# Performance work log

Measured on AMD Instinct MI355X. Metric: run time of the kernel, lower is better.

Reference implementation:

```python
import jax, jax.numpy as jnp
import numpy as np

B, S, D, H, L = 8, 4096, 512, 512, 2


def log_g(x):
    # log of g(x) where g(x) = x + 0.5 for x >= 0 else sigmoid(x)
    return jnp.where(x >= 0, jnp.log(jax.nn.relu(x) + 0.5), -jax.nn.softplus(-x))


def g(x):
    return jnp.where(x >= 0, x + 0.5, jax.nn.sigmoid(x))


def mingru_layer(x, h0, wz, bz, wh, bh):
    """Log-space parallel-scan minGRU layer.
    x: (B,S,Din), h0: (B,1,H) positive (already g-activated).
    wz,wh: (H,Din); bz,bh: (H,). Returns full hidden sequence (B,S,H)."""
    k = jnp.einsum('bsd,hd->bsh', x, wz) + bz          # gate pre-activation
    log_z = -jax.nn.softplus(-k)                        # log sigmoid(k)
    log_coeffs = -jax.nn.softplus(k)                    # log(1 - sigmoid(k))
    log_h_tilde = log_g(jnp.einsum('bsd,hd->bsh', x, wh) + bh)
    log_values = log_z + log_h_tilde                    # log(z * h_tilde)
    log_h0 = jnp.log(h0)                                # (B,1,H)
    # Heinsen associative scan in log space
    a_star = jnp.cumsum(
        jnp.concatenate([jnp.zeros_like(log_h0), log_coeffs], axis=1), axis=1)  # (B,S+1,H)
    log_vals = jnp.concatenate([log_h0, log_values], axis=1)                     # (B,S+1,H)
    log_h = a_star + jax.lax.cumlogsumexp(log_vals - a_star, axis=1)
    return jnp.exp(log_h)[:, 1:]                        # (B,S,H)


def setup_inputs() -> dict:
    key = jax.random.key(0)
    ks = jax.random.split(key, 1 + 4 * L)
    x = jax.random.normal(ks[0], (B, S, D), dtype=jnp.float32)
    inp = {'x': x}
    dims_in = [D] + [H] * (L - 1)
    i = 1
    for l in range(L):
        din = dims_in[l]
        stdv = 1.0 / np.sqrt(din)
        inp[f'wz{l}'] = jax.random.uniform(ks[i], (H, din), minval=-stdv, maxval=stdv); i += 1
        inp[f'bz{l}'] = jax.random.uniform(ks[i], (H,), minval=-stdv, maxval=stdv); i += 1
        inp[f'wh{l}'] = jax.random.uniform(ks[i], (H, din), minval=-stdv, maxval=stdv); i += 1
        inp[f'bh{l}'] = jax.random.uniform(ks[i], (H,), minval=-stdv, maxval=stdv); i += 1
    return inp


def reference(x, wz0, bz0, wh0, bh0, wz1, bz1, wh1, bh1):
    # h is None -> h0 = g(zeros) = 0.5 for every layer
    h0 = jnp.full((B, 1, H), 0.5, dtype=x.dtype)
    params = [(wz0, bz0, wh0, bh0), (wz1, bz1, wh1, bh1)]
    inp = x
    finals = []
    for (wz, bz, wh, bh) in params:
        out = mingru_layer(inp, h0, wz, bz, wh, bh)
        finals.append(out[:, -1:])
        inp = out  # Identity layer transform, no residual, dropout=0
    return out, jnp.stack(finals)  # (B,S,H), (L,B,1,H)
```

## Files before the change

kernel.cpp:

```cpp
#include <hip/hip_runtime.h>
#include <math.h>

#define BB 8
#define SS 4096
#define DD 512
#define HH 512
#define MM (BB*SS)

constexpr int TCH = 64;
constexpr int NC  = SS / TCH;
constexpr int BH  = BB * HH;

constexpr int BM = 128;
constexpr int BN = 64;
constexpr int BK = 64;

typedef short  short8  __attribute__((ext_vector_type(8)));
typedef float  float4v __attribute__((ext_vector_type(4)));

__device__ inline unsigned short f2bf(float f) {
    union { float f; unsigned u; } v; v.f = f;
    unsigned r = v.u + 0x7FFF + ((v.u >> 16) & 1);
    return (unsigned short)(r >> 16);
}
__device__ inline float bf_lo(unsigned u) {
    union { unsigned u; float f; } x; x.u = u << 16; return x.f;
}
__device__ inline float bf_hi(unsigned u) {
    union { unsigned u; float f; } x; x.u = u & 0xffff0000u; return x.f;
}

__device__ inline void async_copy16(const void* g, void* l) {
    __builtin_amdgcn_global_load_lds(
        (const __attribute__((address_space(1))) void*)g,
        (__attribute__((address_space(3))) void*)l, 16, 0, 0);
}

__global__ __launch_bounds__(256)
void conv_bf16(const float* __restrict__ in, short* __restrict__ out) {
    const size_t base = ((size_t)blockIdx.x * 256 + threadIdx.x) * 8;
    float4 a = *(const float4*)(in + base);
    float4 b = *(const float4*)(in + base + 4);
    short8 r;
    r[0] = f2bf(a.x); r[1] = f2bf(a.y); r[2] = f2bf(a.z); r[3] = f2bf(a.w);
    r[4] = f2bf(b.x); r[5] = f2bf(b.y); r[6] = f2bf(b.z); r[7] = f2bf(b.w);
    *(short8*)(out + base) = r;
}

__global__ __launch_bounds__(256)
void conv_bf16_w4(const float* __restrict__ w0, const float* __restrict__ w1,
                  const float* __restrict__ w2, const float* __restrict__ w3,
                  short* __restrict__ out) {
    const float* src = (blockIdx.y == 0) ? w0 : (blockIdx.y == 1) ? w1
                     : (blockIdx.y == 2) ? w2 : w3;
    const size_t base = ((size_t)blockIdx.x * 256 + threadIdx.x) * 8;
    float4 a = *(const float4*)(src + base);
    float4 b = *(const float4*)(src + base + 4);
    short8 r;
    r[0] = f2bf(a.x); r[1] = f2bf(a.y); r[2] = f2bf(a.z); r[3] = f2bf(a.w);
    r[4] = f2bf(b.x); r[5] = f2bf(b.y); r[6] = f2bf(b.z); r[7] = f2bf(b.w);
    *(short8*)(out + (size_t)blockIdx.y * HH * DD + base) = r;
}

__global__ __launch_bounds__(256)
void gemm_gate_mfma(const short* __restrict__ Xg, const short* __restrict__ Wz,
                    const float* __restrict__ bz, const short* __restrict__ Wh,
                    const float* __restrict__ bh, unsigned* __restrict__ AV,
                    float2* __restrict__ cAV)
{
    __shared__ char smem[32768];
    short*    lds    = (short*)smem;
    unsigned* lds_av = (unsigned*)smem;
    constexpr int ZOFF = BM * BK;
    constexpr int HOFF = BM * BK + BN * BK;

    const int t    = threadIdx.x;
    const int wave = t >> 6;
    const int lane = t & 63;
    const int col16 = lane & 15;
    const int quad  = lane >> 4;
    const int wm = wave >> 1;
    const int wn = wave & 1;
    const int m0 = blockIdx.x * BM;
    const int n0 = blockIdx.y * BN;

    float4v accz[4][2], acch[4][2];
    #pragma unroll
    for (int i = 0; i < 4; ++i)
        #pragma unroll
        for (int j = 0; j < 2; ++j) {
            accz[i][j] = (float4v){0.f, 0.f, 0.f, 0.f};
            acch[i][j] = (float4v){0.f, 0.f, 0.f, 0.f};
        }

    const int lr = lane >> 3;
    const int lc = (lane & 7) * 8;

    for (int k0 = 0; k0 < DD; k0 += BK) {
        #pragma unroll
        for (int i = 0; i < 4; ++i) {
            const int r0 = wave * 32 + i * 8;
            async_copy16(Xg + (size_t)(m0 + r0 + lr) * DD + k0 + lc,
                         &lds[r0 * BK]);
        }
        #pragma unroll
        for (int i = 0; i < 2; ++i) {
            const int r0 = wave * 16 + i * 8;
            async_copy16(Wz + (size_t)(n0 + r0 + lr) * DD + k0 + lc,
                         &lds[ZOFF + r0 * BK]);
            async_copy16(Wh + (size_t)(n0 + r0 + lr) * DD + k0 + lc,
                         &lds[HOFF + r0 * BK]);
        }
        __syncthreads();

        #pragma unroll
        for (int kk = 0; kk < 2; ++kk) {
            short8 af[4], bzf[2], bhf[2];
            #pragma unroll
            for (int mi = 0; mi < 4; ++mi)
                af[mi] = *(const short8*)&lds[(wm*64 + mi*16 + col16) * BK + kk*32 + quad*8];
            #pragma unroll
            for (int nj = 0; nj < 2; ++nj) {
                bzf[nj] = *(const short8*)&lds[ZOFF + (wn*32 + nj*16 + col16) * BK + kk*32 + quad*8];
                bhf[nj] = *(const short8*)&lds[HOFF + (wn*32 + nj*16 + col16) * BK + kk*32 + quad*8];
            }
            #pragma unroll
            for (int mi = 0; mi < 4; ++mi)
                #pragma unroll
                for (int nj = 0; nj < 2; ++nj) {
                    accz[mi][nj] = __builtin_amdgcn_mfma_f32_16x16x32_bf16(af[mi], bzf[nj], accz[mi][nj], 0, 0, 0);
                    acch[mi][nj] = __builtin_amdgcn_mfma_f32_16x16x32_bf16(af[mi], bhf[nj], acch[mi][nj], 0, 0, 0);
                }
        }
        __syncthreads();
    }

    #pragma unroll
    for (int nj = 0; nj < 2; ++nj) {
        const int ln = wn*32 + nj*16 + col16;
        const int n  = n0 + ln;
        const float bzn = bz[n], bhn = bh[n];
        #pragma unroll
        for (int mi = 0; mi < 4; ++mi) {
            const int lmb = wm*64 + mi*16 + quad*4;
            #pragma unroll
            for (int reg = 0; reg < 4; ++reg) {
                const float kz = accz[mi][nj][reg] + bzn;
                const float kh = acch[mi][nj][reg] + bhn;
                const float a  = 1.0f / (1.0f + __expf(kz));
                const float ht = (kh >= 0.0f) ? (kh + 0.5f)
                                              : (1.0f / (1.0f + __expf(-kh)));
                const float v  = (1.0f - a) * ht;
                lds_av[(lmb + reg) * 64 + ln] = ((unsigned)f2bf(v) << 16) | f2bf(a);
            }
        }
    }
    __syncthreads();

    {
        const int row0 = t >> 4;
        const int col  = (t & 15) * 4;
        #pragma unroll
        for (int i = 0; i < 8; ++i) {
            const int row = row0 + i * 16;
            const uint4 u = *(const uint4*)&lds_av[row * 64 + col];
            *(uint4*)&AV[(size_t)(m0 + row) * HH + n0 + col] = u;
        }
    }

    if (t < 128) {
        const int c  = t >> 6;
        const int ln = t & 63;
        float prod = 1.0f, hl = 0.0f;
        #pragma unroll 8
        for (int s = 0; s < TCH; ++s) {
            const unsigned u = lds_av[(c * TCH + s) * 64 + ln];
            const float a = bf_lo(u), v = bf_hi(u);
            hl   = fmaf(a, hl, v);
            prod *= a;
        }
        const int b  = m0 >> 12;
        const int cg = ((m0 & 4095) >> 6) + c;
        cAV[(size_t)cg * BH + b * HH + (n0 + ln)] = make_float2(prod, hl);
    }
}

__global__ __launch_bounds__(256)
void scan_apply_f32(const unsigned* __restrict__ AV,
                    const float2* __restrict__ cAV,
                    float* __restrict__ out, float* __restrict__ finals)
{
    const int h = blockIdx.x * 256 + threadIdx.x;
    const int b = blockIdx.y;
    const int c = blockIdx.z;
    const int ch = b * HH + h;
    float hcur = 0.5f;
    for (int cp = 0; cp < c; ++cp) {
        const float2 s = cAV[(size_t)cp * BH + ch];
        hcur = fmaf(s.x, hcur, s.y);
    }
    size_t base = ((size_t)(b * SS + c * TCH)) * HH + h;
    for (int tt = 0; tt < TCH; ++tt) {
        const unsigned u = AV[base];
        hcur = fmaf(bf_lo(u), hcur, bf_hi(u));
        out[base] = hcur;
        base += HH;
    }
    if (c == NC - 1) finals[ch] = hcur;
}

__global__ __launch_bounds__(256)
void scan_apply_bf16(const unsigned* __restrict__ AV,
                     const float2* __restrict__ cAV,
                     short* __restrict__ out, float* __restrict__ finals)
{
    const int h = blockIdx.x * 256 + threadIdx.x;
    const int b = blockIdx.y;
    const int c = blockIdx.z;
    const int ch = b * HH + h;
    float hcur = 0.5f;
    for (int cp = 0; cp < c; ++cp) {
        const float2 s = cAV[(size_t)cp * BH + ch];
        hcur = fmaf(s.x, hcur, s.y);
    }
    size_t base = ((size_t)(b * SS + c * TCH)) * HH + h;
    for (int tt = 0; tt < TCH; ++tt) {
        const unsigned u = AV[base];
        hcur = fmaf(bf_lo(u), hcur, bf_hi(u));
        out[base] = (short)f2bf(hcur);
        base += HH;
    }
    if (c == NC - 1) finals[ch] = hcur;
}

extern "C" void kernel_launch(void* const* d_in, const int* in_sizes, int n_in,
                              void* d_out, int out_size, void* d_ws, size_t ws_size,
                              hipStream_t stream)
{
    const float* x   = (const float*)d_in[0];
    const float* wz0 = (const float*)d_in[1];
    const float* bz0 = (const float*)d_in[2];
    const float* wh0 = (const float*)d_in[3];
    const float* bh0 = (const float*)d_in[4];
    const float* wz1 = (const float*)d_in[5];
    const float* bz1 = (const float*)d_in[6];
    const float* wh1 = (const float*)d_in[7];
    const float* bh1 = (const float*)d_in[8];

    float* out    = (float*)d_out;
    float* finals = out + (size_t)MM * HH;

    unsigned* AV  = (unsigned*)d_ws;
    short* Xbf    = (short*)(AV + (size_t)MM * HH);
    short* Wbf    = Xbf + (size_t)MM * DD;
    float2* cAV   = (float2*)(Wbf + (size_t)4 * HH * DD);

    short* Wz0 = Wbf;
    short* Wh0 = Wbf + (size_t)1 * HH * DD;
    short* Wz1 = Wbf + (size_t)2 * HH * DD;
    short* Wh1 = Wbf + (size_t)3 * HH * DD;

    const dim3 gg(MM / BM, HH / BN);
    const dim3 gs(HH / 256, BB, NC);

    conv_bf16   <<<MM * DD / 8 / 256, 256, 0, stream>>>(x, Xbf);
    conv_bf16_w4<<<dim3(HH * DD / 8 / 256, 4), 256, 0, stream>>>(wz0, wh0, wz1, wh1, Wbf);

    gemm_gate_mfma <<<gg, 256, 0, stream>>>(Xbf, Wz0, bz0, Wh0, bh0, AV, cAV);
    scan_apply_bf16<<<gs, 256, 0, stream>>>(AV, cAV, Xbf, finals);

    gemm_gate_mfma <<<gg, 256, 0, stream>>>(Xbf, Wz1, bz1, Wh1, bh1, AV, cAV);
    scan_apply_f32 <<<gs, 256, 0, stream>>>(AV, cAV, out, finals + BH);
}
```

Measured before the change: 332.4 us.

## Merge conversion kernels, use fast reciprocal, split chunk reduction across all threads

Merges the x and weight bf16 conversion kernels into one launch to save a kernel launch. In the GEMM epilogue, exact divisions are replaced with the hardware reciprocal, and the sigmoid is evaluated without a branch. The per-chunk prefix reduction now uses all 256 threads: each half-chunk is reduced separately and the two are combined with a lane shuffle, which halves the serial loop length. The scan loops also get an unroll pragma. The reciprocal approximation may slightly change numerics.

```diff
diff --git a/kernel.cpp b/kernel.cpp
--- a/kernel.cpp
+++ b/kernel.cpp
@@ -29,6 +29,9 @@
 __device__ inline float bf_hi(unsigned u) {
     union { unsigned u; float f; } x; x.u = u & 0xffff0000u; return x.f;
 }
+__device__ inline float fast_rcp(float x) {
+    return __builtin_amdgcn_rcpf(x);
+}
 
 __device__ inline void async_copy16(const void* g, void* l) {
     __builtin_amdgcn_global_load_lds(
@@ -37,29 +40,31 @@
 }
 
 __global__ __launch_bounds__(256)
-void conv_bf16(const float* __restrict__ in, short* __restrict__ out) {
-    const size_t base = ((size_t)blockIdx.x * 256 + threadIdx.x) * 8;
-    float4 a = *(const float4*)(in + base);
-    float4 b = *(const float4*)(in + base + 4);
-    short8 r;
-    r[0] = f2bf(a.x); r[1] = f2bf(a.y); r[2] = f2bf(a.z); r[3] = f2bf(a.w);
-    r[4] = f2bf(b.x); r[5] = f2bf(b.y); r[6] = f2bf(b.z); r[7] = f2bf(b.w);
-    *(short8*)(out + base) = r;
-}
-
-__global__ __launch_bounds__(256)
-void conv_bf16_w4(const float* __restrict__ w0, const float* __restrict__ w1,
-                  const float* __restrict__ w2, const float* __restrict__ w3,
-                  short* __restrict__ out) {
-    const float* src = (blockIdx.y == 0) ? w0 : (blockIdx.y == 1) ? w1
-                     : (blockIdx.y == 2) ? w2 : w3;
-    const size_t base = ((size_t)blockIdx.x * 256 + threadIdx.x) * 8;
+void conv_all(const float* __restrict__ x,
+              const float* __restrict__ w0, const float* __restrict__ w1,
+              const float* __restrict__ w2, const float* __restrict__ w3,
+              short* __restrict__ Xbf, short* __restrict__ Wbf)
+{
+    constexpr int XBLK = MM * DD / 8 / 256;
+    constexpr int WBLK = HH * DD / 8 / 256;
+    const int bid = blockIdx.x;
+    const float* src; short* dst; size_t base;
+    if (bid < XBLK) {
+        src = x; dst = Xbf;
+        base = ((size_t)bid * 256 + threadIdx.x) * 8;
+    } else {
+        const int idx  = bid - XBLK;
+        const int wsel = idx / WBLK;
+        src = (wsel == 0) ? w0 : (wsel == 1) ? w1 : (wsel == 2) ? w2 : w3;
+        dst = Wbf + (size_t)wsel * HH * DD;
+        base = ((size_t)(idx % WBLK) * 256 + threadIdx.x) * 8;
+    }
     float4 a = *(const float4*)(src + base);
     float4 b = *(const float4*)(src + base + 4);
     short8 r;
     r[0] = f2bf(a.x); r[1] = f2bf(a.y); r[2] = f2bf(a.z); r[3] = f2bf(a.w);
     r[4] = f2bf(b.x); r[5] = f2bf(b.y); r[6] = f2bf(b.z); r[7] = f2bf(b.w);
-    *(short8*)(out + (size_t)blockIdx.y * HH * DD + base) = r;
+    *(short8*)(dst + base) = r;
 }
 
 __global__ __launch_bounds__(256)
@@ -147,9 +152,9 @@
             for (int reg = 0; reg < 4; ++reg) {
                 const float kz = accz[mi][nj][reg] + bzn;
                 const float kh = acch[mi][nj][reg] + bhn;
-                const float a  = 1.0f / (1.0f + __expf(kz));
-                const float ht = (kh >= 0.0f) ? (kh + 0.5f)
-                                              : (1.0f / (1.0f + __expf(-kh)));
+                const float a  = fast_rcp(1.0f + __expf(kz));
+                const float sn = fast_rcp(1.0f + __expf(-kh));
+                const float ht = (kh >= 0.0f) ? (kh + 0.5f) : sn;
                 const float v  = (1.0f - a) * ht;
                 lds_av[(lmb + reg) * 64 + ln] = ((unsigned)f2bf(v) << 16) | f2bf(a);
             }
@@ -168,20 +173,27 @@
         }
     }
 
-    if (t < 128) {
-        const int c  = t >> 6;
-        const int ln = t & 63;
+    {
+        const int task = t >> 1;
+        const int hf   = t & 1;
+        const int c    = task >> 6;
+        const int ln   = task & 63;
         float prod = 1.0f, hl = 0.0f;
         #pragma unroll 8
-        for (int s = 0; s < TCH; ++s) {
-            const unsigned u = lds_av[(c * TCH + s) * 64 + ln];
+        for (int s = 0; s < TCH / 2; ++s) {
+            const unsigned u = lds_av[(c * TCH + hf * 32 + s) * 64 + ln];
             const float a = bf_lo(u), v = bf_hi(u);
             hl   = fmaf(a, hl, v);
             prod *= a;
         }
-        const int b  = m0 >> 12;
-        const int cg = ((m0 & 4095) >> 6) + c;
-        cAV[(size_t)cg * BH + b * HH + (n0 + ln)] = make_float2(prod, hl);
+        const float pA = __shfl_xor(prod, 1);
+        const float pV = __shfl_xor(hl, 1);
+        if (hf == 0) {
+            const int b  = m0 >> 12;
+            const int cg = ((m0 & 4095) >> 6) + c;
+            cAV[(size_t)cg * BH + b * HH + (n0 + ln)] =
+                make_float2(prod * pA, fmaf(pA, hl, pV));
+        }
     }
 }
 
@@ -200,6 +212,7 @@
         hcur = fmaf(s.x, hcur, s.y);
     }
     size_t base = ((size_t)(b * SS + c * TCH)) * HH + h;
+    #pragma unroll 8
     for (int tt = 0; tt < TCH; ++tt) {
         const unsigned u = AV[base];
         hcur = fmaf(bf_lo(u), hcur, bf_hi(u));
@@ -224,6 +237,7 @@
         hcur = fmaf(s.x, hcur, s.y);
     }
     size_t base = ((size_t)(b * SS + c * TCH)) * HH + h;
+    #pragma unroll 8
     for (int tt = 0; tt < TCH; ++tt) {
         const unsigned u = AV[base];
         hcur = fmaf(bf_lo(u), hcur, bf_hi(u));
@@ -263,8 +277,8 @@
     const dim3 gg(MM / BM, HH / BN);
     const dim3 gs(HH / 256, BB, NC);
 
-    conv_bf16   <<<MM * DD / 8 / 256, 256, 0, stream>>>(x, Xbf);
-    conv_bf16_w4<<<dim3(HH * DD / 8 / 256, 4), 256, 0, stream>>>(wz0, wh0, wz1, wh1, Wbf);
+    conv_all<<<MM * DD / 8 / 256 + 4 * (HH * DD / 8 / 256), 256, 0, stream>>>(
+        x, wz0, wh0, wz1, wh1, Xbf, Wbf);
 
     gemm_gate_mfma <<<gg, 256, 0, stream>>>(Xbf, Wz0, bz0, Wh0, bh0, AV, cAV);
     scan_apply_bf16<<<gs, 256, 0, stream>>>(AV, cAV, Xbf, finals);
```

New measurement: 322.7 us. 2.9% less time.
